# Kernel tuning notes

Hardware: AMD Instinct MI355X
Metric: run time of the kernel (lower is better)

## Reference

```python
import jax, jax.numpy as jnp
import numpy as np

VOCAB = 100000
EMB = 128
B = 16384
P = 4
N = 20
EPS = 1e-3


def setup_inputs() -> dict:
    key = jax.random.key(0)
    k1, k2, k3, k4, k5 = jax.random.split(key, 5)
    return {
        "x": jax.random.randint(k1, (B,), 0, VOCAB),
        "positive_samples": jax.random.randint(k2, (B, P), 0, VOCAB),
        "negative_samples": jax.random.randint(k3, (B, N), 0, VOCAB),
        "emb_table": jax.random.normal(k4, (VOCAB, EMB), dtype=jnp.float32) * 0.02,
        "out_weight": jax.random.normal(k5, (VOCAB, EMB), dtype=jnp.float32) * 0.02,
    }


def reference(x, positive_samples, negative_samples, emb_table, out_weight):
    emb = emb_table[x]  # [B, D]
    ctx_w = out_weight[positive_samples]  # [B, P, D] gather
    neg_w = out_weight[negative_samples]  # [B, N, D] gather
    # batched dot products (torch.bmm with emb.unsqueeze(-1))
    pos_logits = jnp.einsum("bpd,bd->bp", ctx_w, emb)
    neg_logits = jnp.einsum("bnd,bd->bn", neg_w, emb)
    pos_out = jax.nn.sigmoid(pos_logits)
    neg_out = jax.nn.sigmoid(neg_logits)
    positive_loss = -jnp.mean(jnp.log(pos_out))
    negative_loss = -jnp.mean(jnp.log(1.0 - neg_out + EPS))
    return positive_loss + negative_loss
```

## Files before the change

### kernel.cpp

```cpp
#include <hip/hip_runtime.h>
#include <math.h>

#define VOCAB 100000
#define EMB 128
#define BATCH 16384
#define NPOS 4
#define NNEG 20
#define EPSV 1e-3f

#define NBLOCKS 2048
#define NTHREADS 256
#define WAVES_PER_BLOCK (NTHREADS / 64)
#define ELEMS_PER_WAVE (BATCH / (NBLOCKS * WAVES_PER_BLOCK))

__global__ __launch_bounds__(NTHREADS) void w2v_main(
    const int* __restrict__ x,
    const int* __restrict__ pos,
    const int* __restrict__ neg,
    const float* __restrict__ emb,
    const float* __restrict__ outw,
    float* __restrict__ partials)
{
    const int tid  = threadIdx.x;
    const int lane = tid & 63;
    const int wid  = tid >> 6;
    const int g    = lane >> 4;
    const int i    = lane & 15;

    const int wv = blockIdx.x * WAVES_PER_BLOCK + wid;

    float pos_acc = 0.0f;
    float neg_acc = 0.0f;

    for (int e = 0; e < ELEMS_PER_WAVE; ++e) {
        const int b  = wv * ELEMS_PER_WAVE + e;
        const int xb = x[b];

        const float4* embr = (const float4*)(emb + (long)xb * EMB);
        const float4 e0 = embr[i * 2];
        const float4 e1 = embr[i * 2 + 1];

        float z0, z1, z2, z3, z4, z5;
#pragma unroll
        for (int iter = 0; iter < 6; ++iter) {
            int sidx;
            if (iter == 0) sidx = pos[b * NPOS + g];
            else           sidx = neg[b * NNEG + (iter - 1) * 4 + g];

            const float4* wr = (const float4*)(outw + (long)sidx * EMB);
            const float4 w0 = wr[i * 2];
            const float4 w1 = wr[i * 2 + 1];

            float p = e0.x * w0.x + e0.y * w0.y + e0.z * w0.z + e0.w * w0.w
                    + e1.x * w1.x + e1.y * w1.y + e1.z * w1.z + e1.w * w1.w;

            p += __shfl_xor(p, 1);
            p += __shfl_xor(p, 2);
            p += __shfl_xor(p, 4);
            p += __shfl_xor(p, 8);

            if      (iter == 0) z0 = p;
            else if (iter == 1) z1 = p;
            else if (iter == 2) z2 = p;
            else if (iter == 3) z3 = p;
            else if (iter == 4) z4 = p;
            else                z5 = p;
        }

        if (i < 6) {
            float z = z0;
            z = (i == 1) ? z1 : z;
            z = (i == 2) ? z2 : z;
            z = (i == 3) ? z3 : z;
            z = (i == 4) ? z4 : z;
            z = (i == 5) ? z5 : z;
            const float t = __expf(-z);
            const float s = 1.0f / (1.0f + t);
            const float v = (i == 0) ? s : (1.0f - s + EPSV);
            const float term = __logf(v);
            if (i == 0) pos_acc += term;
            else        neg_acc += term;
        }
    }

#pragma unroll
    for (int m = 1; m < 64; m <<= 1) {
        pos_acc += __shfl_xor(pos_acc, m);
        neg_acc += __shfl_xor(neg_acc, m);
    }

    __shared__ float sp[WAVES_PER_BLOCK];
    __shared__ float sn[WAVES_PER_BLOCK];
    if (lane == 0) { sp[wid] = pos_acc; sn[wid] = neg_acc; }
    __syncthreads();
    if (tid == 0) {
        float tp = 0.0f, tn = 0.0f;
#pragma unroll
        for (int w = 0; w < WAVES_PER_BLOCK; ++w) { tp += sp[w]; tn += sn[w]; }
        partials[blockIdx.x * 2]     = tp;
        partials[blockIdx.x * 2 + 1] = tn;
    }
}

__global__ __launch_bounds__(256) void w2v_final(
    const float* __restrict__ partials, float* __restrict__ out)
{
    const int tid  = threadIdx.x;
    const int lane = tid & 63;
    const int wid  = tid >> 6;

    float tp = 0.0f, tn = 0.0f;
    for (int k = tid; k < NBLOCKS; k += 256) {
        tp += partials[k * 2];
        tn += partials[k * 2 + 1];
    }
#pragma unroll
    for (int m = 1; m < 64; m <<= 1) {
        tp += __shfl_xor(tp, m);
        tn += __shfl_xor(tn, m);
    }
    __shared__ float sp[4];
    __shared__ float sn[4];
    if (lane == 0) { sp[wid] = tp; sn[wid] = tn; }
    __syncthreads();
    if (tid == 0) {
        float fp = sp[0] + sp[1] + sp[2] + sp[3];
        float fn = sn[0] + sn[1] + sn[2] + sn[3];
        out[0] = -fp / (float)(BATCH * NPOS) - fn / (float)(BATCH * NNEG);
    }
}

extern "C" void kernel_launch(void* const* d_in, const int* in_sizes, int n_in,
                              void* d_out, int out_size, void* d_ws, size_t ws_size,
                              hipStream_t stream) {
    const int*   x    = (const int*)d_in[0];
    const int*   pos  = (const int*)d_in[1];
    const int*   neg  = (const int*)d_in[2];
    const float* emb  = (const float*)d_in[3];
    const float* outw = (const float*)d_in[4];
    float* out = (float*)d_out;
    float* partials = (float*)d_ws;

    w2v_main<<<NBLOCKS, NTHREADS, 0, stream>>>(x, pos, neg, emb, outw, partials);
    w2v_final<<<1, 256, 0, stream>>>(partials, out);
}
```

Before: 38.55 us.

## Fuse final reduction via last-block atomic counter and preload sample indices

```diff
diff --git a/kernel.cpp b/kernel.cpp
--- a/kernel.cpp
+++ b/kernel.cpp
@@ -12,44 +12,50 @@
 #define NTHREADS 256
 #define WAVES_PER_BLOCK (NTHREADS / 64)
 #define ELEMS_PER_WAVE (BATCH / (NBLOCKS * WAVES_PER_BLOCK))
+#define COUNTER_OFF_BYTES 32768
 
-__global__ __launch_bounds__(NTHREADS) void w2v_main(
+__global__ __launch_bounds__(NTHREADS) void w2v_fused(
     const int* __restrict__ x,
     const int* __restrict__ pos,
     const int* __restrict__ neg,
     const float* __restrict__ emb,
     const float* __restrict__ outw,
-    float* __restrict__ partials)
+    float* __restrict__ partials,
+    unsigned int* __restrict__ counter,
+    float* __restrict__ out)
 {
     const int tid  = threadIdx.x;
     const int lane = tid & 63;
     const int wid  = tid >> 6;
     const int g    = lane >> 4;
     const int i    = lane & 15;
-
-    const int wv = blockIdx.x * WAVES_PER_BLOCK + wid;
+    const int wv   = blockIdx.x * WAVES_PER_BLOCK + wid;
 
     float pos_acc = 0.0f;
     float neg_acc = 0.0f;
 
+#pragma unroll
     for (int e = 0; e < ELEMS_PER_WAVE; ++e) {
         const int b  = wv * ELEMS_PER_WAVE + e;
         const int xb = x[b];
 
+        int myidx = 0;
+        if (lane < NPOS)            myidx = pos[b * NPOS + lane];
+        else if (lane < NPOS + NNEG) myidx = neg[b * NNEG + (lane - NPOS)];
+
         const float4* embr = (const float4*)(emb + (long)xb * EMB);
-        const float4 e0 = embr[i * 2];
-        const float4 e1 = embr[i * 2 + 1];
+        const float4 e0 = embr[i];
+        const float4 e1 = embr[i + 16];
 
         float z0, z1, z2, z3, z4, z5;
 #pragma unroll
         for (int iter = 0; iter < 6; ++iter) {
-            int sidx;
-            if (iter == 0) sidx = pos[b * NPOS + g];
-            else           sidx = neg[b * NNEG + (iter - 1) * 4 + g];
+            const int src  = (iter == 0) ? g : (NPOS + (iter - 1) * 4 + g);
+            const int sidx = __shfl(myidx, src);
 
             const float4* wr = (const float4*)(outw + (long)sidx * EMB);
-            const float4 w0 = wr[i * 2];
-            const float4 w1 = wr[i * 2 + 1];
+            const float4 w0 = wr[i];
+            const float4 w1 = wr[i + 16];
 
             float p = e0.x * w0.x + e0.y * w0.y + e0.z * w0.z + e0.w * w0.w
                     + e1.x * w1.x + e1.y * w1.y + e1.z * w1.z + e1.w * w1.w;
@@ -91,42 +97,41 @@
 
     __shared__ float sp[WAVES_PER_BLOCK];
     __shared__ float sn[WAVES_PER_BLOCK];
+    __shared__ int   sLast;
     if (lane == 0) { sp[wid] = pos_acc; sn[wid] = neg_acc; }
     __syncthreads();
     if (tid == 0) {
         float tp = 0.0f, tn = 0.0f;
 #pragma unroll
         for (int w = 0; w < WAVES_PER_BLOCK; ++w) { tp += sp[w]; tn += sn[w]; }
-        partials[blockIdx.x * 2]     = tp;
-        partials[blockIdx.x * 2 + 1] = tn;
+        partials[2 * blockIdx.x]     = tp;
+        partials[2 * blockIdx.x + 1] = tn;
+        __threadfence();
+        const unsigned prev = atomicAdd(counter, 1u);
+        sLast = (prev == NBLOCKS - 1) ? 1 : 0;
     }
-}
+    __syncthreads();
 
-__global__ __launch_bounds__(256) void w2v_final(
-    const float* __restrict__ partials, float* __restrict__ out)
-{
-    const int tid  = threadIdx.x;
-    const int lane = tid & 63;
-    const int wid  = tid >> 6;
-
-    float tp = 0.0f, tn = 0.0f;
-    for (int k = tid; k < NBLOCKS; k += 256) {
-        tp += partials[k * 2];
-        tn += partials[k * 2 + 1];
-    }
+    if (sLast) {
+        __threadfence();
+        volatile const float* vp = partials;
+        float tp = 0.0f, tn = 0.0f;
+        for (int k = tid; k < NBLOCKS; k += NTHREADS) {
+            tp += vp[2 * k];
+            tn += vp[2 * k + 1];
+        }
 #pragma unroll
-    for (int m = 1; m < 64; m <<= 1) {
-        tp += __shfl_xor(tp, m);
-        tn += __shfl_xor(tn, m);
-    }
-    __shared__ float sp[4];
-    __shared__ float sn[4];
-    if (lane == 0) { sp[wid] = tp; sn[wid] = tn; }
-    __syncthreads();
-    if (tid == 0) {
-        float fp = sp[0] + sp[1] + sp[2] + sp[3];
-        float fn = sn[0] + sn[1] + sn[2] + sn[3];
-        out[0] = -fp / (float)(BATCH * NPOS) - fn / (float)(BATCH * NNEG);
+        for (int m = 1; m < 64; m <<= 1) {
+            tp += __shfl_xor(tp, m);
+            tn += __shfl_xor(tn, m);
+        }
+        if (lane == 0) { sp[wid] = tp; sn[wid] = tn; }
+        __syncthreads();
+        if (tid == 0) {
+            const float fp = sp[0] + sp[1] + sp[2] + sp[3];
+            const float fn = sn[0] + sn[1] + sn[2] + sn[3];
+            out[0] = -fp / (float)(BATCH * NPOS) - fn / (float)(BATCH * NNEG);
+        }
     }
 }
 
@@ -139,8 +144,11 @@
     const float* emb  = (const float*)d_in[3];
     const float* outw = (const float*)d_in[4];
     float* out = (float*)d_out;
-    float* partials = (float*)d_ws;
 
-    w2v_main<<<NBLOCKS, NTHREADS, 0, stream>>>(x, pos, neg, emb, outw, partials);
-    w2v_final<<<1, 256, 0, stream>>>(partials, out);
+    float*        partials = (float*)d_ws;
+    unsigned int* counter  = (unsigned int*)((char*)d_ws + COUNTER_OFF_BYTES);
+
+    hipMemsetAsync(counter, 0, sizeof(unsigned int), stream);
+    w2v_fused<<<NBLOCKS, NTHREADS, 0, stream>>>(x, pos, neg, emb, outw,
+                                                partials, counter, out);
 }
```

After: 107.7 us. 179% more time.

## Assign one batch element per wave with all 24 sample indices loaded up front

Applied to the files above, without the earlier changes.

```diff
diff --git a/kernel.cpp b/kernel.cpp
--- a/kernel.cpp
+++ b/kernel.cpp
@@ -6,12 +6,12 @@
 #define BATCH 16384
 #define NPOS 4
 #define NNEG 20
+#define NSAMP (NPOS + NNEG)
 #define EPSV 1e-3f
 
-#define NBLOCKS 2048
+#define NBLOCKS 4096
 #define NTHREADS 256
 #define WAVES_PER_BLOCK (NTHREADS / 64)
-#define ELEMS_PER_WAVE (BATCH / (NBLOCKS * WAVES_PER_BLOCK))
 
 __global__ __launch_bounds__(NTHREADS) void w2v_main(
     const int* __restrict__ x,
@@ -24,63 +24,47 @@
     const int tid  = threadIdx.x;
     const int lane = tid & 63;
     const int wid  = tid >> 6;
-    const int g    = lane >> 4;
-    const int i    = lane & 15;
+    const int half = lane >> 5;
+    const int li   = lane & 31;
 
-    const int wv = blockIdx.x * WAVES_PER_BLOCK + wid;
+    const int b  = blockIdx.x * WAVES_PER_BLOCK + wid;
+    const int xb = x[b];
 
-    float pos_acc = 0.0f;
-    float neg_acc = 0.0f;
+    int myidx = 0;
+    if (lane < NPOS)             myidx = pos[b * NPOS + lane];
+    else if (lane < NSAMP)       myidx = neg[b * NNEG + (lane - NPOS)];
 
-    for (int e = 0; e < ELEMS_PER_WAVE; ++e) {
-        const int b  = wv * ELEMS_PER_WAVE + e;
-        const int xb = x[b];
+    const float4 e = ((const float4*)(emb + (long)xb * EMB))[li];
 
-        const float4* embr = (const float4*)(emb + (long)xb * EMB);
-        const float4 e0 = embr[i * 2];
-        const float4 e1 = embr[i * 2 + 1];
+    float z[12];
+#pragma unroll
+    for (int j = 0; j < 12; ++j) {
+        const int s = __shfl(myidx, 2 * j + half);
+        const float4 w = ((const float4*)(outw + (long)s * EMB))[li];
+        z[j] = e.x * w.x + e.y * w.y + e.z * w.z + e.w * w.w;
+    }
 
-        float z0, z1, z2, z3, z4, z5;
 #pragma unroll
-        for (int iter = 0; iter < 6; ++iter) {
-            int sidx;
-            if (iter == 0) sidx = pos[b * NPOS + g];
-            else           sidx = neg[b * NNEG + (iter - 1) * 4 + g];
+    for (int j = 0; j < 12; ++j) {
+        z[j] += __shfl_xor(z[j], 1);
+        z[j] += __shfl_xor(z[j], 2);
+        z[j] += __shfl_xor(z[j], 4);
+        z[j] += __shfl_xor(z[j], 8);
+        z[j] += __shfl_xor(z[j], 16);
+    }
 
-            const float4* wr = (const float4*)(outw + (long)sidx * EMB);
-            const float4 w0 = wr[i * 2];
-            const float4 w1 = wr[i * 2 + 1];
-
-            float p = e0.x * w0.x + e0.y * w0.y + e0.z * w0.z + e0.w * w0.w
-                    + e1.x * w1.x + e1.y * w1.y + e1.z * w1.z + e1.w * w1.w;
-
-            p += __shfl_xor(p, 1);
-            p += __shfl_xor(p, 2);
-            p += __shfl_xor(p, 4);
-            p += __shfl_xor(p, 8);
-
-            if      (iter == 0) z0 = p;
-            else if (iter == 1) z1 = p;
-            else if (iter == 2) z2 = p;
-            else if (iter == 3) z3 = p;
-            else if (iter == 4) z4 = p;
-            else                z5 = p;
-        }
-
-        if (i < 6) {
-            float z = z0;
-            z = (i == 1) ? z1 : z;
-            z = (i == 2) ? z2 : z;
-            z = (i == 3) ? z3 : z;
-            z = (i == 4) ? z4 : z;
-            z = (i == 5) ? z5 : z;
-            const float t = __expf(-z);
-            const float s = 1.0f / (1.0f + t);
-            const float v = (i == 0) ? s : (1.0f - s + EPSV);
-            const float term = __logf(v);
-            if (i == 0) pos_acc += term;
-            else        neg_acc += term;
-        }
+    float pos_acc = 0.0f, neg_acc = 0.0f;
+    if (li < 12) {
+        float zz = z[0];
+#pragma unroll
+        for (int j = 1; j < 12; ++j) zz = (li == j) ? z[j] : zz;
+        const int s = 2 * li + half;
+        const float t  = __expf(-zz);
+        const float sg = 1.0f / (1.0f + t);
+        const float v  = (s < NPOS) ? sg : (1.0f - sg + EPSV);
+        const float term = __logf(v);
+        if (s < NPOS) pos_acc = term;
+        else          neg_acc = term;
     }
 
 #pragma unroll
@@ -97,12 +81,12 @@
         float tp = 0.0f, tn = 0.0f;
 #pragma unroll
         for (int w = 0; w < WAVES_PER_BLOCK; ++w) { tp += sp[w]; tn += sn[w]; }
-        partials[blockIdx.x * 2]     = tp;
-        partials[blockIdx.x * 2 + 1] = tn;
+        partials[2 * blockIdx.x]     = tp;
+        partials[2 * blockIdx.x + 1] = tn;
     }
 }
 
-__global__ __launch_bounds__(256) void w2v_final(
+__global__ __launch_bounds__(1024) void w2v_final(
     const float* __restrict__ partials, float* __restrict__ out)
 {
     const int tid  = threadIdx.x;
@@ -110,22 +94,23 @@
     const int wid  = tid >> 6;
 
     float tp = 0.0f, tn = 0.0f;
-    for (int k = tid; k < NBLOCKS; k += 256) {
-        tp += partials[k * 2];
-        tn += partials[k * 2 + 1];
+    for (int k = tid; k < NBLOCKS; k += 1024) {
+        tp += partials[2 * k];
+        tn += partials[2 * k + 1];
     }
 #pragma unroll
     for (int m = 1; m < 64; m <<= 1) {
         tp += __shfl_xor(tp, m);
         tn += __shfl_xor(tn, m);
     }
-    __shared__ float sp[4];
-    __shared__ float sn[4];
+    __shared__ float sp[16];
+    __shared__ float sn[16];
     if (lane == 0) { sp[wid] = tp; sn[wid] = tn; }
     __syncthreads();
     if (tid == 0) {
-        float fp = sp[0] + sp[1] + sp[2] + sp[3];
-        float fn = sn[0] + sn[1] + sn[2] + sn[3];
+        float fp = 0.0f, fn = 0.0f;
+#pragma unroll
+        for (int w = 0; w < 16; ++w) { fp += sp[w]; fn += sn[w]; }
         out[0] = -fp / (float)(BATCH * NPOS) - fn / (float)(BATCH * NNEG);
     }
 }
@@ -142,5 +127,5 @@
     float* partials = (float*)d_ws;
 
     w2v_main<<<NBLOCKS, NTHREADS, 0, stream>>>(x, pos, neg, emb, outw, partials);
-    w2v_final<<<1, 256, 0, stream>>>(partials, out);
+    w2v_final<<<1, 1024, 0, stream>>>(partials, out);
 }
```

Result: no change. 38.59 us (+0.1%).
